# Performance work log

Measured on AMD Instinct MI355X. Metric: run time of the kernel, lower is better.

Reference implementation:

```python
import jax, jax.numpy as jnp
import numpy as np

N, P, C, K = 16, 2048, 64, 16
EPS = 1e-5


def _bn(x, gamma, beta, axes):
    # training-mode batchnorm: biased variance over all dims except channel (last)
    m = jnp.mean(x, axis=axes, keepdims=True)
    v = jnp.var(x, axis=axes, keepdims=True)
    return (x - m) * jax.lax.rsqrt(v + EPS) * gamma + beta


def setup_inputs() -> dict:
    key = jax.random.key(0)
    ks = jax.random.split(key, 16)
    w = lambda k, shape: jax.random.normal(k, shape, jnp.float32) * 0.05
    inp = {"features": jax.random.normal(ks[0], (N, C, P), jnp.float32)}
    # edge-conv MLP: layer 0 takes 2*C input channels
    inp["w0"], inp["b0"] = w(ks[1], (C, 2 * C)), jnp.zeros((C,), jnp.float32)
    inp["g0"], inp["be0"] = jnp.ones((C,), jnp.float32), jnp.zeros((C,), jnp.float32)
    inp["w1"], inp["b1"] = w(ks[2], (C, C)), jnp.zeros((C,), jnp.float32)
    inp["g1"], inp["be1"] = jnp.ones((C,), jnp.float32), jnp.zeros((C,), jnp.float32)
    inp["w2"], inp["b2"] = w(ks[3], (C, C)), jnp.zeros((C,), jnp.float32)
    inp["g2"], inp["be2"] = jnp.ones((C,), jnp.float32), jnp.zeros((C,), jnp.float32)
    # shortcut 1x1 conv + BN
    inp["ws"], inp["bs"] = w(ks[4], (C, C)), jnp.zeros((C,), jnp.float32)
    inp["gs"], inp["bes"] = jnp.ones((C,), jnp.float32), jnp.zeros((C,), jnp.float32)
    return inp


def reference(features, w0, b0, g0, be0, w1, b1, g1, be1, w2, b2, g2, be2, ws, bs, gs, bes):
    # index != 0: features come in as (N, C, P) -> (N, P, C)
    X = jnp.transpose(features, (0, 2, 1))  # (N, P, C)

    # --- KNN via full pairwise squared distances ---
    r = jnp.sum(X * X, axis=-1)  # (N, P)
    d = r[:, :, None] - 2.0 * jnp.einsum('npc,nqc->npq', X, X) + r[:, None, :]
    _, idx = jax.lax.top_k(-d, K + 1)
    idx = idx[:, :, 1:]  # drop self, (N, P, K)

    # --- irregular gather + edge-feature concat ---
    f = X[jnp.arange(X.shape[0])[:, None, None], idx]  # (N, P, K, C)
    fc = jnp.broadcast_to(X[:, :, None, :], f.shape)   # center feature tiled
    h = jnp.concatenate([fc, fc - f], axis=-1)         # (N, P, K, 2C)

    def conv_bn_relu(h, w, b, g, be):
        h = jnp.einsum('npki,oi->npko', h, w) + b
        return jax.nn.relu(_bn(h, g, be, (0, 1, 2)))

    h = conv_bn_relu(h, w0, b0, g0, be0)
    h = conv_bn_relu(h, w1, b1, g1, be1)
    h = conv_bn_relu(h, w2, b2, g2, be2)
    h = jnp.mean(h, axis=2)  # aggregate over K -> (N, P, C)

    # shortcut: 1x1 conv + BN on center features
    sc = jnp.einsum('npi,oi->npo', X, ws) + bs
    sc = _bn(sc, gs, bes, (0, 1))

    out = jax.nn.relu(h + sc)           # (N, P, C)
    return jnp.transpose(out, (0, 2, 1))  # (N, C, P) to match torch layout
```

## Files before the change

### kernel.cpp

```cpp
#include <hip/hip_runtime.h>

using u16    = unsigned short;
using u64    = unsigned long long;
using bf16x8 = __attribute__((ext_vector_type(8))) short;
using f32x4  = __attribute__((ext_vector_type(4))) float;
using u16x4  = __attribute__((ext_vector_type(4))) u16;

#define NB   16
#define PP   2048
#define CC   64
#define KK   16
#define MROWS (NB*PP*KK)
#define NPTS  (NB*PP)

__device__ __forceinline__ float b2f(u16 u) { return __uint_as_float(((unsigned)u) << 16); }
__device__ __forceinline__ u16 f2b(float f) {
  unsigned u = __float_as_uint(f);
  return (u16)((u + 0x7fffu + ((u >> 16) & 1u)) >> 16);
}

__device__ __forceinline__ u64 dkey(float d, int qi) {
  unsigned u = __float_as_uint(d);
  u = u ^ (((unsigned)((int)u >> 31)) | 0x80000000u);
  return ((u64)u << 32) | (unsigned)qi;
}

template<bool UP>
__device__ __forceinline__ void ce(u64 &a, u64 &b) {
  const bool lt = a < b;
  const u64 lo = lt ? a : b;
  const u64 hi = lt ? b : a;
  if (UP) { a = lo; b = hi; } else { a = hi; b = lo; }
}

__device__ __forceinline__ void sort16(u64 (&v)[16]) {
  #pragma unroll
  for (int k = 2; k <= 16; k <<= 1) {
    #pragma unroll
    for (int j = k >> 1; j > 0; j >>= 1) {
      #pragma unroll
      for (int i = 0; i < 16; ++i) {
        const int l = i ^ j;
        if (l > i) {
          if ((i & k) == 0) ce<true>(v[i], v[l]);
          else              ce<false>(v[i], v[l]);
        }
      }
    }
  }
}

__device__ __forceinline__ void merge16(u64 (&dl)[16], const u64 (&nb)[16]) {
  u64 t[16];
  #pragma unroll
  for (int s = 0; s < 16; ++s) {
    const u64 a = dl[s], b = nb[15 - s];
    t[s] = a < b ? a : b;
  }
  #pragma unroll
  for (int j = 8; j > 0; j >>= 1) {
    #pragma unroll
    for (int i = 0; i < 16; ++i) {
      const int l = i ^ j;
      if (l > i) ce<true>(t[i], t[l]);
    }
  }
  #pragma unroll
  for (int s = 0; s < 16; ++s) dl[s] = t[s];
}

__global__ __launch_bounds__(256) void prep_k(const float* __restrict__ F,
                                              float* __restrict__ X,
                                              u16* __restrict__ Xb,
                                              float* __restrict__ r) {
  int gidx = blockIdx.x * 256 + threadIdx.x;
  int n = gidx >> 11, p = gidx & 2047;
  const float* src = F + (size_t)n * CC * PP + p;
  float v[CC];
  float rr = 0.f;
  #pragma unroll
  for (int c = 0; c < CC; ++c) { v[c] = src[(size_t)c * PP]; rr += v[c] * v[c]; }
  float* dst = X + (size_t)gidx * CC;
  #pragma unroll
  for (int c = 0; c < CC; c += 4) {
    float4 w; w.x = v[c]; w.y = v[c+1]; w.z = v[c+2]; w.w = v[c+3];
    *(float4*)(dst + c) = w;
  }
  u16* db = Xb + (size_t)gidx * CC;
  #pragma unroll
  for (int c = 0; c < CC; c += 8) {
    bf16x8 w8;
    #pragma unroll
    for (int j = 0; j < 8; ++j) w8[j] = (short)f2b(v[c + j]);
    *(bf16x8*)(db + c) = w8;
  }
  r[gidx] = rr;
}

__global__ __launch_bounds__(256) void cvtw_k(const float* __restrict__ w0, const float* __restrict__ w1,
                                              const float* __restrict__ w2, const float* __restrict__ wsb,
                                              u16* __restrict__ b0, u16* __restrict__ b1,
                                              u16* __restrict__ b2, u16* __restrict__ bs) {
  int i = blockIdx.x * 256 + threadIdx.x;
  if (i < 8192)        b0[i]          = f2b(w0[i]);
  else if (i < 12288)  b1[i - 8192]   = f2b(w1[i - 8192]);
  else if (i < 16384)  b2[i - 12288]  = f2b(w2[i - 12288]);
  else if (i < 20480)  bs[i - 16384]  = f2b(wsb[i - 16384]);
}

__global__ __launch_bounds__(256, 3) void knn_k(const float* __restrict__ X,
                                                const float* __restrict__ r,
                                                int* __restrict__ idx) {
  __shared__ float lds[12800];
  float* Xp = lds;
  float* Xq = lds + 4352;

  const int n  = blockIdx.x >> 5;
  const int pb = (blockIdx.x & 31) * 64;
  const int t  = threadIdx.x;
  const float* Xn = X + (size_t)n * PP * CC;
  const float* rb = r + (size_t)n * PP;

  const int ph   = t >> 5;
  const int qh   = t & 31;
  const int prow = t & 63;
  const int qh2  = t >> 6;
  const int u4   = (prow & 7) * 4;

  {
    const int pr = t & 63, ct = t >> 6;
    const float* src = Xn + (size_t)(pb + pr) * CC + ct * 16;
    #pragma unroll
    for (int j = 0; j < 16; j += 4) {
      float4 v = *(const float4*)(src + j);
      Xp[(ct*16 + j + 0) * 68 + pr] = v.x;
      Xp[(ct*16 + j + 1) * 68 + pr] = v.y;
      Xp[(ct*16 + j + 2) * 68 + pr] = v.z;
      Xp[(ct*16 + j + 3) * 68 + pr] = v.w;
    }
  }

  u64 dl[16];
  #pragma unroll
  for (int s = 0; s < 16; ++s) dl[s] = ~0ULL;

  #pragma unroll 1
  for (int qb = 0; qb < PP; qb += 128) {
    __syncthreads();
    {
      const int qr = t & 127, hf = t >> 7;
      const float* src = Xn + (size_t)(qb + qr) * CC + hf * 32;
      #pragma unroll
      for (int j = 0; j < 32; j += 4) {
        float4 v = *(const float4*)(src + j);
        Xq[(hf*32 + j + 0) * 132 + qr] = v.x;
        Xq[(hf*32 + j + 1) * 132 + qr] = v.y;
        Xq[(hf*32 + j + 2) * 132 + qr] = v.z;
        Xq[(hf*32 + j + 3) * 132 + qr] = v.w;
      }
    }
    __syncthreads();

    float acc[8][4];
    #pragma unroll
    for (int i = 0; i < 8; ++i)
      #pragma unroll
      for (int j = 0; j < 4; ++j) acc[i][j] = 0.f;

    #pragma unroll 4
    for (int c = 0; c < 64; ++c) {
      const float4 a0 = *(const float4*)&Xp[c*68 + ph*8];
      const float4 a1 = *(const float4*)&Xp[c*68 + ph*8 + 4];
      const float4 bq = *(const float4*)&Xq[c*132 + qh*4];
      float av[8] = {a0.x, a0.y, a0.z, a0.w, a1.x, a1.y, a1.z, a1.w};
      float bv[4] = {bq.x, bq.y, bq.z, bq.w};
      #pragma unroll
      for (int i = 0; i < 8; ++i)
        #pragma unroll
        for (int j = 0; j < 4; ++j)
          acc[i][j] = fmaf(av[i], bv[j], acc[i][j]);
    }
    __syncthreads();

    {
      const int qg0 = qb + qh*4;
      const float4 rv = *(const float4*)(rb + qg0);
      #pragma unroll
      for (int i = 0; i < 8; ++i) {
        const int p  = ph*8 + i;
        const int pg = pb + p;
        float d0 = rv.x - 2.f * acc[i][0]; if (qg0 + 0 == pg) d0 = 3.0e38f;
        float d1 = rv.y - 2.f * acc[i][1]; if (qg0 + 1 == pg) d1 = 3.0e38f;
        float d2 = rv.z - 2.f * acc[i][2]; if (qg0 + 2 == pg) d2 = 3.0e38f;
        float d3 = rv.w - 2.f * acc[i][3]; if (qg0 + 3 == pg) d3 = 3.0e38f;
        float4 dv; dv.x = d0; dv.y = d1; dv.z = d2; dv.w = d3;
        *(float4*)&Xq[(size_t)p * 132 + ((qh ^ (i*4)) * 4)] = dv;
      }
    }
    __syncthreads();

    #pragma unroll
    for (int half = 0; half < 2; ++half) {
      u64 nb[16];
      #pragma unroll
      for (int bi = 0; bi < 4; ++bi) {
        const int b = qh2*8 + half*4 + bi;
        const float4 dv = *(const float4*)&Xq[(size_t)prow * 132 + ((b ^ u4) * 4)];
        const int qg = qb + b*4;
        nb[bi*4+0] = dkey(dv.x, qg+0);
        nb[bi*4+1] = dkey(dv.y, qg+1);
        nb[bi*4+2] = dkey(dv.z, qg+2);
        nb[bi*4+3] = dkey(dv.w, qg+3);
      }
      sort16(nb);
      merge16(dl, nb);
    }
  }

  __syncthreads();
  {
    u64* mb = (u64*)Xq;
    #pragma unroll
    for (int s = 0; s < 16; ++s) mb[s * 256 + t] = dl[s];
  }
  __syncthreads();
  if (t < 64) {
    const u64* mb = (const u64*)Xq;
    #pragma unroll 1
    for (int j = 1; j < 4; ++j) {
      u64 nb[16];
      #pragma unroll
      for (int s = 0; s < 16; ++s) nb[s] = mb[s * 256 + (t + 64 * j)];
      merge16(dl, nb);
    }
    #pragma unroll
    for (int s = 0; s < 16; ++s)
      idx[((size_t)n * PP + pb + t) * KK + s] = (int)(dl[s] & 0xFFFFFFFFu);
  }
}

template<int KIN, bool GATHER, bool BNRELU>
__global__ __launch_bounds__(256) void conv_k(const u16* __restrict__ in,
                                              const int* __restrict__ idxp,
                                              const u16* __restrict__ wb,
                                              const float* __restrict__ bias,
                                              const float* __restrict__ st,
                                              u16* __restrict__ yout,
                                              float* __restrict__ partials) {
  constexpr int NKB = KIN / 32;
  __shared__ float sred[4][4][32];
  const int t = threadIdx.x;
  const int wv = t >> 6, l = t & 63, hi = l >> 4, lo = l & 15;
  const int rbase = blockIdx.x * 256 + wv * 64;

  bf16x8 wf[4][NKB];
  #pragma unroll
  for (int ob = 0; ob < 4; ++ob)
    #pragma unroll
    for (int kb = 0; kb < NKB; ++kb)
      wf[ob][kb] = *(const bf16x8*)(wb + (size_t)(ob*16 + lo) * KIN + kb*32 + hi*8);

  int qv[4];
  if constexpr (GATHER) {
    #pragma unroll
    for (int rb = 0; rb < 4; ++rb) {
      const int g = (rbase + rb*16) >> 4;
      qv[rb] = idxp[g * KK + lo];
    }
  }

  f32x4 acc[4][4];
  #pragma unroll
  for (int a = 0; a < 4; ++a)
    #pragma unroll
    for (int b = 0; b < 4; ++b) { f32x4 z = {0.f, 0.f, 0.f, 0.f}; acc[a][b] = z; }

  #pragma unroll
  for (int kb = 0; kb < NKB; ++kb) {
    float sv[8], tv[8];
    if constexpr (BNRELU) {
      const int k0 = kb*32 + hi*8;
      *(float4*)&sv[0] = *(const float4*)(st + k0);
      *(float4*)&sv[4] = *(const float4*)(st + k0 + 4);
      *(float4*)&tv[0] = *(const float4*)(st + KIN + k0);
      *(float4*)&tv[4] = *(const float4*)(st + KIN + k0 + 4);
    }
    bf16x8 af[4];
    #pragma unroll
    for (int rb = 0; rb < 4; ++rb) {
      if constexpr (GATHER) {
        const int g  = (rbase + rb*16) >> 4;
        const int k0 = kb*32 + hi*8;
        const bf16x8 fc = *(const bf16x8*)(in + (size_t)g * CC + (k0 & 63));
        if (kb < 2) {
          af[rb] = fc;
        } else {
          const int nn = g >> 11;
          const bf16x8 fv = *(const bf16x8*)(in + (size_t)(nn * PP + qv[rb]) * CC + (k0 & 63));
          bf16x8 df;
          #pragma unroll
          for (int j = 0; j < 8; ++j)
            df[j] = (short)f2b(b2f((u16)fc[j]) - b2f((u16)fv[j]));
          af[rb] = df;
        }
      } else {
        const int row = rbase + rb*16 + lo;
        const bf16x8 rv = *(const bf16x8*)(in + (size_t)row * KIN + kb*32 + hi*8);
        if constexpr (BNRELU) {
          bf16x8 tr;
          #pragma unroll
          for (int j = 0; j < 8; ++j) {
            const float x = fmaxf(b2f((u16)rv[j]) * sv[j] + tv[j], 0.f);
            tr[j] = (short)f2b(x);
          }
          af[rb] = tr;
        } else {
          af[rb] = rv;
        }
      }
    }
    #pragma unroll
    for (int ob = 0; ob < 4; ++ob)
      #pragma unroll
      for (int rb = 0; rb < 4; ++rb)
        acc[rb][ob] = __builtin_amdgcn_mfma_f32_16x16x32_bf16(wf[ob][kb], af[rb], acc[rb][ob], 0, 0, 0);
  }

  float ssum[16], qsum[16];
  #pragma unroll
  for (int j = 0; j < 16; ++j) { ssum[j] = 0.f; qsum[j] = 0.f; }
  #pragma unroll
  for (int ob = 0; ob < 4; ++ob) {
    const int o0 = ob*16 + hi*4;
    const float4 bv = *(const float4*)(bias + o0);
    #pragma unroll
    for (int rb = 0; rb < 4; ++rb) {
      const int row = rbase + rb*16 + lo;
      const float v0 = acc[rb][ob][0] + bv.x;
      const float v1 = acc[rb][ob][1] + bv.y;
      const float v2 = acc[rb][ob][2] + bv.z;
      const float v3 = acc[rb][ob][3] + bv.w;
      u16x4 pk; pk[0] = f2b(v0); pk[1] = f2b(v1); pk[2] = f2b(v2); pk[3] = f2b(v3);
      *(u16x4*)(yout + (size_t)row * CC + o0) = pk;
      ssum[ob*4+0] += v0; qsum[ob*4+0] += v0*v0;
      ssum[ob*4+1] += v1; qsum[ob*4+1] += v1*v1;
      ssum[ob*4+2] += v2; qsum[ob*4+2] += v2*v2;
      ssum[ob*4+3] += v3; qsum[ob*4+3] += v3*v3;
    }
  }
  #pragma unroll
  for (int m = 1; m < 16; m <<= 1) {
    #pragma unroll
    for (int j = 0; j < 16; ++j) {
      ssum[j] += __shfl_xor(ssum[j], m, 64);
      qsum[j] += __shfl_xor(qsum[j], m, 64);
    }
  }
  if (lo == 0) {
    #pragma unroll
    for (int j = 0; j < 16; ++j) {
      sred[wv][hi][j*2]   = ssum[j];
      sred[wv][hi][j*2+1] = qsum[j];
    }
  }
  __syncthreads();
  if (t < 128) {
    const int c = t & 63, half = t >> 6;
    const int slot = ((c >> 4) * 4 + (c & 3)) * 2 + half;
    const int h2 = (c >> 2) & 3;
    const float v = sred[0][h2][slot] + sred[1][h2][slot] + sred[2][h2][slot] + sred[3][h2][slot];
    partials[(size_t)blockIdx.x * 128 + half * 64 + c] = v;
  }
}

__global__ __launch_bounds__(256) void red1_k(const float* __restrict__ partials,
                                              float* __restrict__ out, int nwg) {
  __shared__ float accs[2][128];
  const int t = threadIdx.x, e = t & 127, h = t >> 7;
  float s = 0.f;
  for (int w = blockIdx.x + h * 64; w < nwg; w += 128)
    s += partials[(size_t)w * 128 + e];
  accs[h][e] = s;
  __syncthreads();
  if (t < 128) out[(size_t)blockIdx.x * 128 + t] = accs[0][t] + accs[1][t];
}

__global__ __launch_bounds__(128) void red2_k(const float* __restrict__ p2,
                                              const float* __restrict__ g,
                                              const float* __restrict__ be,
                                              float* __restrict__ st, float invM) {
  __shared__ float sq[128];
  const int t = threadIdx.x;
  float s = 0.f;
  #pragma unroll 8
  for (int w = 0; w < 64; ++w) s += p2[w * 128 + t];
  sq[t] = s;
  __syncthreads();
  if (t < 64) {
    const float S = sq[t], Q = sq[64 + t];
    const float m = S * invM;
    const float v = fmaxf(Q * invM - m * m, 0.f);
    const float sc = g[t] * rsqrtf(v + 1e-5f);
    st[t] = sc;
    st[64 + t] = be[t] - m * sc;
  }
}

__global__ __launch_bounds__(256) void final_k(const u16* __restrict__ y2,
                                               const u16* __restrict__ ysc,
                                               const float* __restrict__ st2,
                                               const float* __restrict__ stS,
                                               float* __restrict__ out) {
  __shared__ float ot[64][68];
  const int b = blockIdx.x, t = threadIdx.x;
  const int n = b >> 5, p0 = (b & 31) * 64;
  const int phh = t >> 2, jh = t & 3, c0 = jh * 16;
  const int g = n * PP + p0 + phh;
  float acc[16];
  #pragma unroll
  for (int i = 0; i < 16; ++i) acc[i] = 0.f;
  float sv[16], tv[16];
  #pragma unroll
  for (int i = 0; i < 16; ++i) { sv[i] = st2[c0 + i]; tv[i] = st2[64 + c0 + i]; }
  for (int k = 0; k < KK; ++k) {
    const u16* rp = y2 + ((size_t)g * KK + k) * CC + c0;
    const bf16x8 v0 = *(const bf16x8*)rp;
    const bf16x8 v1 = *(const bf16x8*)(rp + 8);
    #pragma unroll
    for (int j = 0; j < 8; ++j) {
      acc[j]     += fmaxf(b2f((u16)v0[j]) * sv[j]     + tv[j],     0.f);
      acc[8 + j] += fmaxf(b2f((u16)v1[j]) * sv[8 + j] + tv[8 + j], 0.f);
    }
  }
  const u16* sp = ysc + (size_t)g * CC + c0;
  const bf16x8 s0 = *(const bf16x8*)sp;
  const bf16x8 s1 = *(const bf16x8*)(sp + 8);
  #pragma unroll
  for (int i = 0; i < 16; ++i) {
    const float scx = b2f((u16)(i < 8 ? s0[i] : s1[i - 8])) * stS[c0 + i] + stS[64 + c0 + i];
    ot[c0 + i][phh] = fmaxf(acc[i] * (1.f / 16.f) + scx, 0.f);
  }
  __syncthreads();
  const int c = t >> 2, pc = t & 3;
  const float* src = &ot[c][pc * 16];
  float* dst = out + (size_t)n * CC * PP + (size_t)c * PP + p0 + pc * 16;
  #pragma unroll
  for (int j = 0; j < 16; j += 4) *(float4*)(dst + j) = *(const float4*)(src + j);
}

extern "C" void kernel_launch(void* const* d_in, const int* in_sizes, int n_in,
                              void* d_out, int out_size, void* d_ws, size_t ws_size,
                              hipStream_t stream) {
  (void)in_sizes; (void)n_in; (void)out_size; (void)ws_size;
  const float* F   = (const float*)d_in[0];
  const float* w0  = (const float*)d_in[1];
  const float* b0  = (const float*)d_in[2];
  const float* g0  = (const float*)d_in[3];
  const float* be0 = (const float*)d_in[4];
  const float* w1  = (const float*)d_in[5];
  const float* b1  = (const float*)d_in[6];
  const float* g1  = (const float*)d_in[7];
  const float* be1 = (const float*)d_in[8];
  const float* w2  = (const float*)d_in[9];
  const float* b2  = (const float*)d_in[10];
  const float* g2  = (const float*)d_in[11];
  const float* be2 = (const float*)d_in[12];
  const float* wS  = (const float*)d_in[13];
  const float* bS  = (const float*)d_in[14];
  const float* gS  = (const float*)d_in[15];
  const float* beS = (const float*)d_in[16];

  char* ws = (char*)d_ws;
  size_t off = 0;
  auto carve = [&](size_t bytes) -> void* {
    void* p = ws + off;
    off += (bytes + 255) & ~(size_t)255;
    return p;
  };
  float* X        = (float*)carve((size_t)NPTS * CC * 4);
  u16*   Xb       = (u16*)  carve((size_t)NPTS * CC * 2);
  float* rr       = (float*)carve((size_t)NPTS * 4);
  int*   idx      = (int*)  carve((size_t)NPTS * KK * 4);
  u16*   wb0      = (u16*)  carve(8192 * 2);
  u16*   wb1      = (u16*)  carve(4096 * 2);
  u16*   wb2      = (u16*)  carve(4096 * 2);
  u16*   wbs      = (u16*)  carve(4096 * 2);
  u16*   y        = (u16*)  carve((size_t)MROWS * CC * 2);
  u16*   ysc      = (u16*)  carve((size_t)NPTS * CC * 2);
  float* partials = (float*)carve((size_t)2048 * 128 * 4);
  float* p2       = (float*)carve((size_t)64 * 128 * 4);
  float* st0      = (float*)carve(128 * 4);
  float* st1      = (float*)carve(128 * 4);
  float* st2      = (float*)carve(128 * 4);
  float* stS      = (float*)carve(128 * 4);

  prep_k<<<NPTS / 256, 256, 0, stream>>>(F, X, Xb, rr);
  cvtw_k<<<80, 256, 0, stream>>>(w0, w1, w2, wS, wb0, wb1, wb2, wbs);
  knn_k<<<NB * (PP / 64), 256, 0, stream>>>(X, rr, idx);

  conv_k<128, true,  false><<<MROWS / 256, 256, 0, stream>>>(Xb, idx, wb0, b0, nullptr, y, partials);
  red1_k<<<64, 256, 0, stream>>>(partials, p2, MROWS / 256);
  red2_k<<<1, 128, 0, stream>>>(p2, g0, be0, st0, 1.f / (float)MROWS);

  conv_k<64, false, true><<<MROWS / 256, 256, 0, stream>>>(y, nullptr, wb1, b1, st0, y, partials);
  red1_k<<<64, 256, 0, stream>>>(partials, p2, MROWS / 256);
  red2_k<<<1, 128, 0, stream>>>(p2, g1, be1, st1, 1.f / (float)MROWS);

  conv_k<64, false, true><<<MROWS / 256, 256, 0, stream>>>(y, nullptr, wb2, b2, st1, y, partials);
  red1_k<<<64, 256, 0, stream>>>(partials, p2, MROWS / 256);
  red2_k<<<1, 128, 0, stream>>>(p2, g2, be2, st2, 1.f / (float)MROWS);

  conv_k<64, false, false><<<NPTS / 256, 256, 0, stream>>>(Xb, nullptr, wbs, bS, nullptr, ysc, partials);
  red1_k<<<64, 256, 0, stream>>>(partials, p2, NPTS / 256);
  red2_k<<<1, 128, 0, stream>>>(p2, gS, beS, stS, 1.f / (float)NPTS);

  final_k<<<NB * (PP / 64), 256, 0, stream>>>(y, ysc, st2, stS, (float*)d_out);
}
```

Baseline: 429.3 us.

## Double KNN block threads to 512 and split per-thread tile and merge work

The KNN kernel now runs 512 threads per block. Each thread computes a 4x4 distance tile instead of 8x4 and sorts and merges one 16-candidate batch per query tile instead of two. A two-stage LDS reduction combines the 8 per-row candidate lists before output. The aim is more latency hiding and more parallelism in the sort/merge stage, which dominates this kernel. In exchange there are more barriers and an extra merge level, and the register budget per thread is tighter under launch bounds of 512 with 4 blocks.

```diff
diff --git a/kernel.cpp b/kernel.cpp
--- a/kernel.cpp
+++ b/kernel.cpp
@@ -108,7 +108,7 @@
   else if (i < 20480)  bs[i - 16384]  = f2b(wsb[i - 16384]);
 }
 
-__global__ __launch_bounds__(256, 3) void knn_k(const float* __restrict__ X,
+__global__ __launch_bounds__(512, 4) void knn_k(const float* __restrict__ X,
                                                 const float* __restrict__ r,
                                                 int* __restrict__ idx) {
   __shared__ float lds[12800];
@@ -121,22 +121,22 @@
   const float* Xn = X + (size_t)n * PP * CC;
   const float* rb = r + (size_t)n * PP;
 
-  const int ph   = t >> 5;
   const int qh   = t & 31;
+  const int pg   = t >> 5;
   const int prow = t & 63;
-  const int qh2  = t >> 6;
+  const int w8   = t >> 6;
   const int u4   = (prow & 7) * 4;
 
   {
     const int pr = t & 63, ct = t >> 6;
-    const float* src = Xn + (size_t)(pb + pr) * CC + ct * 16;
-    #pragma unroll
-    for (int j = 0; j < 16; j += 4) {
+    const float* src = Xn + (size_t)(pb + pr) * CC + ct * 8;
+    #pragma unroll
+    for (int j = 0; j < 8; j += 4) {
       float4 v = *(const float4*)(src + j);
-      Xp[(ct*16 + j + 0) * 68 + pr] = v.x;
-      Xp[(ct*16 + j + 1) * 68 + pr] = v.y;
-      Xp[(ct*16 + j + 2) * 68 + pr] = v.z;
-      Xp[(ct*16 + j + 3) * 68 + pr] = v.w;
+      Xp[(ct*8 + j + 0) * 68 + pr] = v.x;
+      Xp[(ct*8 + j + 1) * 68 + pr] = v.y;
+      Xp[(ct*8 + j + 2) * 68 + pr] = v.z;
+      Xp[(ct*8 + j + 3) * 68 + pr] = v.w;
     }
   }
 
@@ -148,34 +148,33 @@
   for (int qb = 0; qb < PP; qb += 128) {
     __syncthreads();
     {
-      const int qr = t & 127, hf = t >> 7;
-      const float* src = Xn + (size_t)(qb + qr) * CC + hf * 32;
-      #pragma unroll
-      for (int j = 0; j < 32; j += 4) {
+      const int qr = t >> 2, ch = (t & 3) * 16;
+      const float* src = Xn + (size_t)(qb + qr) * CC + ch;
+      #pragma unroll
+      for (int j = 0; j < 16; j += 4) {
         float4 v = *(const float4*)(src + j);
-        Xq[(hf*32 + j + 0) * 132 + qr] = v.x;
-        Xq[(hf*32 + j + 1) * 132 + qr] = v.y;
-        Xq[(hf*32 + j + 2) * 132 + qr] = v.z;
-        Xq[(hf*32 + j + 3) * 132 + qr] = v.w;
+        Xq[(ch + j + 0) * 132 + qr] = v.x;
+        Xq[(ch + j + 1) * 132 + qr] = v.y;
+        Xq[(ch + j + 2) * 132 + qr] = v.z;
+        Xq[(ch + j + 3) * 132 + qr] = v.w;
       }
     }
     __syncthreads();
 
-    float acc[8][4];
-    #pragma unroll
-    for (int i = 0; i < 8; ++i)
+    float acc[4][4];
+    #pragma unroll
+    for (int i = 0; i < 4; ++i)
       #pragma unroll
       for (int j = 0; j < 4; ++j) acc[i][j] = 0.f;
 
     #pragma unroll 4
     for (int c = 0; c < 64; ++c) {
-      const float4 a0 = *(const float4*)&Xp[c*68 + ph*8];
-      const float4 a1 = *(const float4*)&Xp[c*68 + ph*8 + 4];
+      const float4 a = *(const float4*)&Xp[c*68 + pg*4];
       const float4 bq = *(const float4*)&Xq[c*132 + qh*4];
-      float av[8] = {a0.x, a0.y, a0.z, a0.w, a1.x, a1.y, a1.z, a1.w};
+      float av[4] = {a.x, a.y, a.z, a.w};
       float bv[4] = {bq.x, bq.y, bq.z, bq.w};
       #pragma unroll
-      for (int i = 0; i < 8; ++i)
+      for (int i = 0; i < 4; ++i)
         #pragma unroll
         for (int j = 0; j < 4; ++j)
           acc[i][j] = fmaf(av[i], bv[j], acc[i][j]);
@@ -186,31 +185,30 @@
       const int qg0 = qb + qh*4;
       const float4 rv = *(const float4*)(rb + qg0);
       #pragma unroll
-      for (int i = 0; i < 8; ++i) {
-        const int p  = ph*8 + i;
-        const int pg = pb + p;
-        float d0 = rv.x - 2.f * acc[i][0]; if (qg0 + 0 == pg) d0 = 3.0e38f;
-        float d1 = rv.y - 2.f * acc[i][1]; if (qg0 + 1 == pg) d1 = 3.0e38f;
-        float d2 = rv.z - 2.f * acc[i][2]; if (qg0 + 2 == pg) d2 = 3.0e38f;
-        float d3 = rv.w - 2.f * acc[i][3]; if (qg0 + 3 == pg) d3 = 3.0e38f;
+      for (int i = 0; i < 4; ++i) {
+        const int p  = pg*4 + i;
+        const int pgl = pb + p;
+        float d0 = rv.x - 2.f * acc[i][0]; if (qg0 + 0 == pgl) d0 = 3.0e38f;
+        float d1 = rv.y - 2.f * acc[i][1]; if (qg0 + 1 == pgl) d1 = 3.0e38f;
+        float d2 = rv.z - 2.f * acc[i][2]; if (qg0 + 2 == pgl) d2 = 3.0e38f;
+        float d3 = rv.w - 2.f * acc[i][3]; if (qg0 + 3 == pgl) d3 = 3.0e38f;
         float4 dv; dv.x = d0; dv.y = d1; dv.z = d2; dv.w = d3;
-        *(float4*)&Xq[(size_t)p * 132 + ((qh ^ (i*4)) * 4)] = dv;
+        *(float4*)&Xq[(size_t)p * 132 + ((qh ^ ((p & 7) * 4)) * 4)] = dv;
       }
     }
     __syncthreads();
 
-    #pragma unroll
-    for (int half = 0; half < 2; ++half) {
+    {
       u64 nb[16];
       #pragma unroll
-      for (int bi = 0; bi < 4; ++bi) {
-        const int b = qh2*8 + half*4 + bi;
+      for (int bb = 0; bb < 4; ++bb) {
+        const int b = w8*4 + bb;
         const float4 dv = *(const float4*)&Xq[(size_t)prow * 132 + ((b ^ u4) * 4)];
         const int qg = qb + b*4;
-        nb[bi*4+0] = dkey(dv.x, qg+0);
-        nb[bi*4+1] = dkey(dv.y, qg+1);
-        nb[bi*4+2] = dkey(dv.z, qg+2);
-        nb[bi*4+3] = dkey(dv.w, qg+3);
+        nb[bb*4+0] = dkey(dv.x, qg+0);
+        nb[bb*4+1] = dkey(dv.y, qg+1);
+        nb[bb*4+2] = dkey(dv.z, qg+2);
+        nb[bb*4+3] = dkey(dv.w, qg+3);
       }
       sort16(nb);
       merge16(dl, nb);
@@ -219,23 +217,36 @@
 
   __syncthreads();
   {
-    u64* mb = (u64*)Xq;
-    #pragma unroll
-    for (int s = 0; s < 16; ++s) mb[s * 256 + t] = dl[s];
-  }
-  __syncthreads();
-  if (t < 64) {
-    const u64* mb = (const u64*)Xq;
-    #pragma unroll 1
-    for (int j = 1; j < 4; ++j) {
+    u64* mb = (u64*)lds;
+    if (t >= 256) {
+      #pragma unroll
+      for (int s = 0; s < 16; ++s) mb[s * 256 + (t - 256)] = dl[s];
+    }
+    __syncthreads();
+    if (t < 256) {
       u64 nb[16];
       #pragma unroll
-      for (int s = 0; s < 16; ++s) nb[s] = mb[s * 256 + (t + 64 * j)];
+      for (int s = 0; s < 16; ++s) nb[s] = mb[s * 256 + t];
       merge16(dl, nb);
     }
-    #pragma unroll
-    for (int s = 0; s < 16; ++s)
-      idx[((size_t)n * PP + pb + t) * KK + s] = (int)(dl[s] & 0xFFFFFFFFu);
+    __syncthreads();
+    if (t < 256) {
+      #pragma unroll
+      for (int s = 0; s < 16; ++s) mb[s * 256 + t] = dl[s];
+    }
+    __syncthreads();
+    if (t < 64) {
+      #pragma unroll 1
+      for (int j = 1; j < 4; ++j) {
+        u64 nb[16];
+        #pragma unroll
+        for (int s = 0; s < 16; ++s) nb[s] = mb[s * 256 + (t + 64 * j)];
+        merge16(dl, nb);
+      }
+      #pragma unroll
+      for (int s = 0; s < 16; ++s)
+        idx[((size_t)n * PP + pb + t) * KK + s] = (int)(dl[s] & 0xFFFFFFFFu);
+    }
   }
 }
 
@@ -496,7 +507,7 @@
 
   prep_k<<<NPTS / 256, 256, 0, stream>>>(F, X, Xb, rr);
   cvtw_k<<<80, 256, 0, stream>>>(w0, w1, w2, wS, wb0, wb1, wb2, wbs);
-  knn_k<<<NB * (PP / 64), 256, 0, stream>>>(X, rr, idx);
+  knn_k<<<NB * (PP / 64), 512, 0, stream>>>(X, rr, idx);
 
   conv_k<128, true,  false><<<MROWS / 256, 256, 0, stream>>>(Xb, idx, wb0, b0, nullptr, y, partials);
   red1_k<<<64, 256, 0, stream>>>(partials, p2, MROWS / 256);
```

After: 421.3 us. No clear change (-1.9%).
